# Kernel tuning notes

Hardware: AMD Instinct MI355X
Metric: run time of the kernel (lower is better)

The kernel has to match this reference:

```python
import jax, jax.numpy as jnp
import numpy as np

B, IN, OUT = 256, 1024, 1024

def leaky_clamp(x, lo, hi, slope):
    return jnp.where(x < lo, lo + slope * (x - lo),
           jnp.where(x > hi, hi + slope * (x - hi), x))

def setup_inputs() -> dict:
    key = jax.random.key(0)
    kx, kw = jax.random.split(key)
    x = jax.random.normal(kx, (B, IN), dtype=jnp.float32)
    # xavier_normal for (out,in): std = sqrt(2/(in+out))
    std = np.sqrt(2.0 / (IN + OUT)).astype(np.float32)
    weight = jax.random.normal(kw, (OUT, IN), dtype=jnp.float32) * std
    log_tau = jnp.zeros((), dtype=jnp.float32)
    return {"x": x, "weight": weight, "log_tau": log_tau}

def reference(x, weight, log_tau):
    # actual_weight = leaky_clamp(weight, 0, 1, 0.1)
    aw = leaky_clamp(weight, 0.0, 1.0, 0.1)          # (OUT, IN)
    tau = jnp.exp(log_tau)                            # scalar
    z = x[:, None, :] * aw[None, :, :]                # (B, OUT, IN)
    p = jax.nn.softmax(tau * z, axis=-1)              # (B, OUT, IN)
    s = jnp.sum(p * z, axis=-1)                       # (B, OUT)
    return s
```

## Files before the change

### kernel.cpp

```cpp
#include <hip/hip_runtime.h>

#define BB   256
#define IN_  1024
#define OUTN 1024

#define TB  16
#define TO  16
#define KC  256
#define NS  (IN_ / KC)
#define PAD 4

#define LOG2E 1.4426950408889634f

typedef float v2f __attribute__((ext_vector_type(2)));
typedef float v4f __attribute__((ext_vector_type(4)));

__device__ __forceinline__ v2f pk_mul(v2f a, v2f b) {
    v2f d; asm("v_pk_mul_f32 %0, %1, %2" : "=v"(d) : "v"(a), "v"(b)); return d;
}
__device__ __forceinline__ v2f pk_add(v2f a, v2f b) {
    v2f d; asm("v_pk_add_f32 %0, %1, %2" : "=v"(d) : "v"(a), "v"(b)); return d;
}
__device__ __forceinline__ v2f pk_fma(v2f a, v2f b, v2f c) {
    v2f d; asm("v_pk_fma_f32 %0, %1, %2, %3" : "=v"(d) : "v"(a), "v"(b), "v"(c)); return d;
}

__device__ __forceinline__ void lds_barrier() {
    asm volatile("s_waitcnt lgkmcnt(0)\n\ts_barrier" ::: "memory");
}

__device__ __forceinline__ float leaky_clamp01(float v) {
    return __builtin_amdgcn_fmed3f(v, 0.1f * v, fmaf(0.1f, v, 0.9f));
}

__global__ __launch_bounds__(256, 4)
void esm_fused_kernel(const float* __restrict__ x,
                      const float* __restrict__ w,
                      const float* __restrict__ log_tau,
                      float* __restrict__ out) {
    __shared__ float xs[TB][KC + PAD];
    __shared__ float wls[TO][KC + PAD];

    const int tid = threadIdx.x;
    const int bid = blockIdx.x;
    const int bt = bid >> 6;
    const int ot = bid & 63;
    const int b0 = bt * TB;
    const int o0 = ot * TO;

    const float scale = __expf(log_tau[0]) * LOG2E;

    const int tx = tid & 15;
    const int ty = tid >> 4;

    const int srow = tid >> 6;
    const int si4  = (tid & 63) << 2;

    float4 rx[4], rw[4];
    #pragma unroll
    for (int t = 0; t < 4; ++t) {
        const int row = srow + t * 4;
        rx[t] = *(const float4*)&x[(size_t)(b0 + row) * IN_ + si4];
        rw[t] = *(const float4*)&w[(size_t)(o0 + row) * IN_ + si4];
    }

    v2f d0 = {0.f, 0.f}, d1 = {0.f, 0.f};
    v2f n0 = {0.f, 0.f}, n1 = {0.f, 0.f};

    #pragma unroll
    for (int s = 0; s < NS; ++s) {
        if (s) lds_barrier();
        #pragma unroll
        for (int t = 0; t < 4; ++t) {
            const int row = srow + t * 4;
            const float4 xv = rx[t];
            float4 xo;
            xo.x = xv.x * scale; xo.y = xv.y * scale;
            xo.z = xv.z * scale; xo.w = xv.w * scale;
            *(float4*)&xs[row][si4] = xo;
            const float4 wv = rw[t];
            float4 wo;
            wo.x = leaky_clamp01(wv.x); wo.y = leaky_clamp01(wv.y);
            wo.z = leaky_clamp01(wv.z); wo.w = leaky_clamp01(wv.w);
            *(float4*)&wls[row][si4] = wo;
        }
        if (s + 1 < NS) {
            const int i0n = (s + 1) * KC;
            #pragma unroll
            for (int t = 0; t < 4; ++t) {
                const int row = srow + t * 4;
                rx[t] = *(const float4*)&x[(size_t)(b0 + row) * IN_ + i0n + si4];
                rw[t] = *(const float4*)&w[(size_t)(o0 + row) * IN_ + i0n + si4];
            }
        }
        lds_barrier();

        #pragma unroll 4
        for (int i = 0; i < KC; i += 4) {
            const v4f xa = *(const v4f*)&xs[ty][i];
            const v4f wa = *(const v4f*)&wls[tx][i];
            const v2f xl = __builtin_shufflevector(xa, xa, 0, 1);
            const v2f xh = __builtin_shufflevector(xa, xa, 2, 3);
            const v2f wl = __builtin_shufflevector(wa, wa, 0, 1);
            const v2f wh = __builtin_shufflevector(wa, wa, 2, 3);
            const v2f t0 = pk_mul(xl, wl);
            const v2f t1 = pk_mul(xh, wh);
            v2f e0, e1;
            e0.x = __builtin_amdgcn_exp2f(t0.x);
            e0.y = __builtin_amdgcn_exp2f(t0.y);
            e1.x = __builtin_amdgcn_exp2f(t1.x);
            e1.y = __builtin_amdgcn_exp2f(t1.y);
            d0 = pk_add(d0, e0);
            d1 = pk_add(d1, e1);
            n0 = pk_fma(e0, t0, n0);
            n1 = pk_fma(e1, t1, n1);
        }
    }

    const float dsum = (d0.x + d0.y) + (d1.x + d1.y);
    const float nsum = (n0.x + n0.y) + (n1.x + n1.y);
    out[(size_t)(b0 + ty) * OUTN + o0 + tx] = nsum / (dsum * scale);
}

extern "C" void kernel_launch(void* const* d_in, const int* in_sizes, int n_in,
                              void* d_out, int out_size, void* d_ws, size_t ws_size,
                              hipStream_t stream) {
    const float* x  = (const float*)d_in[0];
    const float* w  = (const float*)d_in[1];
    const float* lt = (const float*)d_in[2];
    float* out = (float*)d_out;

    esm_fused_kernel<<<(BB / TB) * (OUTN / TO), 256, 0, stream>>>(x, w, lt, out);
}
```

Before: 93.36 us.

## Use 2x2 register tiles with K-split across wavefronts and LDS reduction

Each thread now computes a 2x2 block of (batch, out) outputs over a quarter of the K range instead of one output over the full range. The goal is to cut LDS reads per exp from two floats to one, since each loaded x and w vector is reused twice. The four K-quarter partial sums are then combined through LDS at the end, which costs an extra barrier and a reduction step. The packed-FP32 inline asm is replaced with scalar math, and the custom barriers are replaced with __syncthreads.

```diff
diff --git a/kernel.cpp b/kernel.cpp
--- a/kernel.cpp
+++ b/kernel.cpp
@@ -12,22 +12,7 @@
 
 #define LOG2E 1.4426950408889634f
 
-typedef float v2f __attribute__((ext_vector_type(2)));
 typedef float v4f __attribute__((ext_vector_type(4)));
-
-__device__ __forceinline__ v2f pk_mul(v2f a, v2f b) {
-    v2f d; asm("v_pk_mul_f32 %0, %1, %2" : "=v"(d) : "v"(a), "v"(b)); return d;
-}
-__device__ __forceinline__ v2f pk_add(v2f a, v2f b) {
-    v2f d; asm("v_pk_add_f32 %0, %1, %2" : "=v"(d) : "v"(a), "v"(b)); return d;
-}
-__device__ __forceinline__ v2f pk_fma(v2f a, v2f b, v2f c) {
-    v2f d; asm("v_pk_fma_f32 %0, %1, %2, %3" : "=v"(d) : "v"(a), "v"(b), "v"(c)); return d;
-}
-
-__device__ __forceinline__ void lds_barrier() {
-    asm volatile("s_waitcnt lgkmcnt(0)\n\ts_barrier" ::: "memory");
-}
 
 __device__ __forceinline__ float leaky_clamp01(float v) {
     return __builtin_amdgcn_fmed3f(v, 0.1f * v, fmaf(0.1f, v, 0.9f));
@@ -50,8 +35,11 @@
 
     const float scale = __expf(log_tau[0]) * LOG2E;
 
-    const int tx = tid & 15;
-    const int ty = tid >> 4;
+    const int h    = tid >> 6;
+    const int cell = tid & 63;
+    const int tx   = cell & 7;
+    const int ty   = cell >> 3;
+    const int ih   = h << 2;
 
     const int srow = tid >> 6;
     const int si4  = (tid & 63) << 2;
@@ -64,12 +52,12 @@
         rw[t] = *(const float4*)&w[(size_t)(o0 + row) * IN_ + si4];
     }
 
-    v2f d0 = {0.f, 0.f}, d1 = {0.f, 0.f};
-    v2f n0 = {0.f, 0.f}, n1 = {0.f, 0.f};
+    float d00 = 0.f, d01 = 0.f, d10 = 0.f, d11 = 0.f;
+    float n00 = 0.f, n01 = 0.f, n10 = 0.f, n11 = 0.f;
 
     #pragma unroll
     for (int s = 0; s < NS; ++s) {
-        if (s) lds_barrier();
+        if (s) __syncthreads();
         #pragma unroll
         for (int t = 0; t < 4; ++t) {
             const int row = srow + t * 4;
@@ -84,6 +72,7 @@
             wo.z = leaky_clamp01(wv.z); wo.w = leaky_clamp01(wv.w);
             *(float4*)&wls[row][si4] = wo;
         }
+        __syncthreads();
         if (s + 1 < NS) {
             const int i0n = (s + 1) * KC;
             #pragma unroll
@@ -93,33 +82,64 @@
                 rw[t] = *(const float4*)&w[(size_t)(o0 + row) * IN_ + i0n + si4];
             }
         }
-        lds_barrier();
 
         #pragma unroll 4
-        for (int i = 0; i < KC; i += 4) {
-            const v4f xa = *(const v4f*)&xs[ty][i];
-            const v4f wa = *(const v4f*)&wls[tx][i];
-            const v2f xl = __builtin_shufflevector(xa, xa, 0, 1);
-            const v2f xh = __builtin_shufflevector(xa, xa, 2, 3);
-            const v2f wl = __builtin_shufflevector(wa, wa, 0, 1);
-            const v2f wh = __builtin_shufflevector(wa, wa, 2, 3);
-            const v2f t0 = pk_mul(xl, wl);
-            const v2f t1 = pk_mul(xh, wh);
-            v2f e0, e1;
-            e0.x = __builtin_amdgcn_exp2f(t0.x);
-            e0.y = __builtin_amdgcn_exp2f(t0.y);
-            e1.x = __builtin_amdgcn_exp2f(t1.x);
-            e1.y = __builtin_amdgcn_exp2f(t1.y);
-            d0 = pk_add(d0, e0);
-            d1 = pk_add(d1, e1);
-            n0 = pk_fma(e0, t0, n0);
-            n1 = pk_fma(e1, t1, n1);
+        for (int m = 0; m < KC / 16; ++m) {
+            const int ib = 16 * m + ih;
+            const v4f xa0 = *(const v4f*)&xs[2 * ty][ib];
+            const v4f xa1 = *(const v4f*)&xs[2 * ty + 1][ib];
+            const v4f wa0 = *(const v4f*)&wls[2 * tx][ib];
+            const v4f wa1 = *(const v4f*)&wls[2 * tx + 1][ib];
+            #pragma unroll
+            for (int k = 0; k < 4; ++k) {
+                const float t00 = xa0[k] * wa0[k];
+                const float t01 = xa0[k] * wa1[k];
+                const float t10 = xa1[k] * wa0[k];
+                const float t11 = xa1[k] * wa1[k];
+                const float e00 = __builtin_amdgcn_exp2f(t00);
+                const float e01 = __builtin_amdgcn_exp2f(t01);
+                const float e10 = __builtin_amdgcn_exp2f(t10);
+                const float e11 = __builtin_amdgcn_exp2f(t11);
+                d00 += e00; d01 += e01; d10 += e10; d11 += e11;
+                n00 = fmaf(e00, t00, n00);
+                n01 = fmaf(e01, t01, n01);
+                n10 = fmaf(e10, t10, n10);
+                n11 = fmaf(e11, t11, n11);
+            }
         }
     }
 
-    const float dsum = (d0.x + d0.y) + (d1.x + d1.y);
-    const float nsum = (n0.x + n0.y) + (n1.x + n1.y);
-    out[(size_t)(b0 + ty) * OUTN + o0 + tx] = nsum / (dsum * scale);
+    __syncthreads();
+    float* sd = &xs[0][0];
+    float* sn = &wls[0][0];
+    const int co00 = (2 * ty) * 16 + 2 * tx;
+    sd[(h << 8) + co00]      = d00;
+    sd[(h << 8) + co00 + 1]  = d01;
+    sd[(h << 8) + co00 + 16] = d10;
+    sd[(h << 8) + co00 + 17] = d11;
+    sn[(h << 8) + co00]      = n00;
+    sn[(h << 8) + co00 + 1]  = n01;
+    sn[(h << 8) + co00 + 16] = n10;
+    sn[(h << 8) + co00 + 17] = n11;
+    __syncthreads();
+    if (h == 0) {
+        float dt00 = 0.f, dt01 = 0.f, dt10 = 0.f, dt11 = 0.f;
+        float nt00 = 0.f, nt01 = 0.f, nt10 = 0.f, nt11 = 0.f;
+        #pragma unroll
+        for (int hh = 0; hh < 4; ++hh) {
+            const int base = (hh << 8) + co00;
+            dt00 += sd[base];      dt01 += sd[base + 1];
+            dt10 += sd[base + 16]; dt11 += sd[base + 17];
+            nt00 += sn[base];      nt01 += sn[base + 1];
+            nt10 += sn[base + 16]; nt11 += sn[base + 17];
+        }
+        const size_t r0o = (size_t)(b0 + 2 * ty) * OUTN + o0 + 2 * tx;
+        const size_t r1o = (size_t)(b0 + 2 * ty + 1) * OUTN + o0 + 2 * tx;
+        out[r0o]     = nt00 / (dt00 * scale);
+        out[r0o + 1] = nt01 / (dt01 * scale);
+        out[r1o]     = nt10 / (dt10 * scale);
+        out[r1o + 1] = nt11 / (dt11 * scale);
+    }
 }
 
 extern "C" void kernel_launch(void* const* d_in, const int* in_sizes, int n_in,
```

Result: no change. 94.04 us (+0.7%).
